# Kernel optimization log

Hardware: AMD Instinct MI355X
Metric: run time of the kernel (lower is better)

Reference implementation:

```python
import jax, jax.numpy as jnp
import numpy as np

INPUT_DIM = 64
INNER_DIM = 64
BATCH = 32768


def setup_inputs() -> dict:
    key = jax.random.key(0)
    ks = jax.random.split(key, 9)
    D, I = INPUT_DIM, INNER_DIM
    s1 = 1.0  # Linear(1, inner): fan_in=1
    s2 = 1.0 / np.sqrt(I)
    sg1 = 1.0 / np.sqrt(D * I)
    sg2 = 1.0 / np.sqrt(I)
    return {
        "x": jax.random.normal(ks[0], (BATCH, D), dtype=jnp.float32),
        # per-feature psi params, stacked over feature dim D
        "W1": jax.random.uniform(ks[1], (D, I), jnp.float32, -s1, s1),   # Linear(1, inner) weight
        "b1": jax.random.uniform(ks[2], (D, I), jnp.float32, -s1, s1),
        "W2": jax.random.uniform(ks[3], (D, I, I), jnp.float32, -s2, s2),  # Linear(inner, inner)
        "b2": jax.random.uniform(ks[4], (D, I), jnp.float32, -s2, s2),
        # g params
        "Wg1": jax.random.uniform(ks[5], (D * I, I), jnp.float32, -sg1, sg1),
        "bg1": jax.random.uniform(ks[6], (I,), jnp.float32, -sg1, sg1),
        "Wg2": jax.random.uniform(ks[7], (I, 1), jnp.float32, -sg2, sg2),
        "bg2": jax.random.uniform(ks[8], (1,), jnp.float32, -sg2, sg2),
    }


def reference(x, W1, b1, W2, b2, Wg1, bg1, Wg2, bg2):
    B = x.shape[0]
    # all psi_i first layers as one broadcasted outer product: [B, D, I]
    h = jnp.tanh(x[:, :, None] * W1[None, :, :] + b1[None, :, :])
    # per-feature second Linear(inner, inner): batched matmul over D
    psi = jnp.einsum("bdi,dio->bdo", h, W2) + b2[None, :, :]
    psi_concat = psi.reshape(B, -1)  # [B, D*I] == torch.cat over features
    hg = jnp.tanh(psi_concat @ Wg1 + bg1)
    out = hg @ Wg2 + bg2  # [B, 1]
    return out
```

## Files before the change

### kernel.cpp

```cpp
#include <hip/hip_runtime.h>
#include <stdint.h>

#define BATCH 32768
#define TANH_C 2.8853900817779268f

typedef __attribute__((ext_vector_type(8))) short short8;
typedef __attribute__((ext_vector_type(4))) float f32x4;
typedef __attribute__((ext_vector_type(16))) float f32x16;
typedef __attribute__((ext_vector_type(4))) unsigned int u32x4;

__device__ __forceinline__ uint16_t bf16_rtne(float f) {
    union { float f; uint32_t u; } v; v.f = f;
    uint32_t u = v.u;
    u += 0x7fffu + ((u >> 16) & 1u);
    return (uint16_t)(u >> 16);
}

#if defined(__has_builtin)
#if __has_builtin(__builtin_amdgcn_cvt_pk_bf16_f32)
#define HAVE_CVT_PK_BF16 1
#endif
#endif

__device__ __forceinline__ uint32_t pack2_bf16(float a, float b) {
#ifdef HAVE_CVT_PK_BF16
    auto v = __builtin_amdgcn_cvt_pk_bf16_f32(a, b);
    uint32_t r; __builtin_memcpy(&r, &v, 4); return r;
#else
    return (uint32_t)bf16_rtne(a) | ((uint32_t)bf16_rtne(b) << 16);
#endif
}

__device__ __forceinline__ uint32_t tanh2_pack(float a, float b) {
    float ea = __builtin_amdgcn_exp2f(a);
    float eb = __builtin_amdgcn_exp2f(b);
    float da = 1.0f + ea, db = 1.0f + eb;
    float ir = __builtin_amdgcn_rcpf(da * db);
    float ha = fmaf(-2.0f * db, ir, 1.0f);
    float hb = fmaf(-2.0f * da, ir, 1.0f);
    return pack2_bf16(ha, hb);
}

__device__ __forceinline__ float fast_tanh(float x) {
    float e = __builtin_amdgcn_exp2f(x * TANH_C);
    return 1.0f - 2.0f * __builtin_amdgcn_rcpf(1.0f + e);
}

__global__ __launch_bounds__(512) void kol_pack(const float* __restrict__ W2,
                                                const float* __restrict__ Wg1,
                                                const float* __restrict__ b2,
                                                uint16_t* __restrict__ Bp,
                                                float* __restrict__ cgpart) {
    __shared__ __align__(16) float w2t[64 * 65];
    __shared__ __align__(16) float g1s[64 * 64];

    const int t = threadIdx.x;
    const int d = blockIdx.x;

    for (int f = t * 4; f < 4096; f += 2048) {
        float4 v = *(const float4*)&W2[(size_t)d * 4096 + f];
        int j = f >> 6, o = f & 63;
        w2t[(o + 0) * 65 + j] = v.x;
        w2t[(o + 1) * 65 + j] = v.y;
        w2t[(o + 2) * 65 + j] = v.z;
        w2t[(o + 3) * 65 + j] = v.w;
        *(float4*)&g1s[f] = *(const float4*)&Wg1[(size_t)d * 4096 + f];
    }
    __syncthreads();

    const int jg = t >> 6;
    const int n  = t & 63;
    float acc[8];
#pragma unroll
    for (int i = 0; i < 8; ++i) acc[i] = 0.f;

#pragma unroll 4
    for (int o = 0; o < 64; ++o) {
        float g = g1s[o * 64 + n];
        const float* w = &w2t[o * 65 + jg * 8];
#pragma unroll
        for (int jj = 0; jj < 8; ++jj) acc[jj] = fmaf(w[jj], g, acc[jj]);
    }

    u32x4 pk;
    pk.x = pack2_bf16(acc[0], acc[1]);
    pk.y = pack2_bf16(acc[2], acc[3]);
    pk.z = pack2_bf16(acc[4], acc[5]);
    pk.w = pack2_bf16(acc[6], acc[7]);
    int off = ((d * 4 + (jg >> 1)) * 2 + (n >> 5)) * 64 + ((jg & 1) << 5) + (n & 31);
    ((u32x4*)Bp)[off] = pk;

    if (t < 64) {
        float a = 0.f;
        const float* b2d = &b2[(size_t)d * 64];
#pragma unroll 4
        for (int o = 0; o < 64; ++o)
            a = fmaf(b2d[o], g1s[o * 64 + t], a);
        cgpart[d * 64 + t] = a;
    }
}

__global__ __launch_bounds__(256) void kol_reduce_cg(const float* __restrict__ cgpart,
                                                     const float* __restrict__ bg1,
                                                     float* __restrict__ cg) {
    __shared__ float red[4][64];
    const int t = threadIdx.x;
    const int n = t & 63, seg = t >> 6;
    float a = 0.f;
#pragma unroll 4
    for (int d = seg * 16; d < seg * 16 + 16; ++d)
        a += cgpart[d * 64 + n];
    red[seg][n] = a;
    __syncthreads();
    if (t < 64)
        cg[n] = bg1[n] + red[0][n] + red[1][n] + red[2][n] + red[3][n];
}

__global__ __launch_bounds__(512, 4) void kol_main(
    const float* __restrict__ x, const float* __restrict__ W1, const float* __restrict__ b1,
    const uint16_t* __restrict__ Bp, const float* __restrict__ cg,
    const float* __restrict__ Wg2, const float* __restrict__ bg2f,
    float* __restrict__ out) {
    __shared__ __align__(16) float smem[12544];
    float* xs  = smem;
    float* w1s = smem + 4352;
    float* b1s = smem + 8448;

    const int tid = threadIdx.x;
    const int wave = tid >> 6, lane = tid & 63;
    const int nn = lane & 31, hi = lane >> 5;
    const int rg = wave & 1, kq = wave >> 1;
    const int rowbase = blockIdx.x * 64;

#pragma unroll
    for (int ff = 0; ff < 2; ++ff) {
        int f = tid * 4 + ff * 2048;
        int r = f >> 6, c = f & 63;
        float4 v = *(const float4*)&x[(size_t)(rowbase + r) * 64 + c];
        v.x *= TANH_C; v.y *= TANH_C; v.z *= TANH_C; v.w *= TANH_C;
        *(float4*)&xs[r * 68 + c] = v;
        *(float4*)&w1s[f] = *(const float4*)&W1[f];
        float4 b = *(const float4*)&b1[f];
        b.x *= TANH_C; b.y *= TANH_C; b.z *= TANH_C; b.w *= TANH_C;
        *(float4*)&b1s[f] = b;
    }
    __syncthreads();

    f32x16 acc0 = {0.f}, acc1 = {0.f};
#pragma unroll
    for (int i = 0; i < 16; ++i) { acc0[i] = 0.f; acc1[i] = 0.f; }

    const u32x4* bp = (const u32x4*)Bp + lane;
    const float* xcol = &xs[(rg * 32 + nn) * 68];

#pragma unroll 2
    for (int dd = 0; dd < 16; ++dd) {
        const int d = kq * 16 + dd;
        const u32x4* bfp = bp + (size_t)d * 512;
        u32x4 bfr[8];
#pragma unroll
        for (int i = 0; i < 8; ++i) bfr[i] = bfp[i * 64];

        const float xv = xcol[d];
        short8 afr[4];
#pragma unroll
        for (int c = 0; c < 4; ++c) {
            const float* wq = &w1s[d * 64 + c * 16 + hi * 8];
            const float* bq = &b1s[d * 64 + c * 16 + hi * 8];
            float4 w0 = *(const float4*)&wq[0];
            float4 w1v = *(const float4*)&wq[4];
            float4 b0 = *(const float4*)&bq[0];
            float4 b1v = *(const float4*)&bq[4];
            union { short8 s; uint32_t u[4]; } a;
            a.u[0] = tanh2_pack(fmaf(xv, w0.x, b0.x), fmaf(xv, w0.y, b0.y));
            a.u[1] = tanh2_pack(fmaf(xv, w0.z, b0.z), fmaf(xv, w0.w, b0.w));
            a.u[2] = tanh2_pack(fmaf(xv, w1v.x, b1v.x), fmaf(xv, w1v.y, b1v.y));
            a.u[3] = tanh2_pack(fmaf(xv, w1v.z, b1v.z), fmaf(xv, w1v.w, b1v.w));
            afr[c] = a.s;
        }
#pragma unroll
        for (int c = 0; c < 4; ++c) {
            union { u32x4 u; short8 s; } b0c, b1c;
            b0c.u = bfr[c * 2 + 0];
            b1c.u = bfr[c * 2 + 1];
            acc0 = __builtin_amdgcn_mfma_f32_32x32x16_bf16(afr[c], b0c.s, acc0, 0, 0, 0);
            acc1 = __builtin_amdgcn_mfma_f32_32x32x16_bf16(afr[c], b1c.s, acc1, 0, 0, 0);
        }
    }

    __syncthreads();
    f32x4* cmb = (f32x4*)smem;
    if (kq != 0) {
        const int widx = (kq - 1) * 2 + rg;
#pragma unroll
        for (int s = 0; s < 8; ++s) {
            const int base = (s & 3) * 4;
            f32x4 v;
            if (s < 4) v = (f32x4){acc0[base], acc0[base + 1], acc0[base + 2], acc0[base + 3]};
            else       v = (f32x4){acc1[base], acc1[base + 1], acc1[base + 2], acc1[base + 3]};
            cmb[(s * 6 + widx) * 64 + lane] = v;
        }
    }
    __syncthreads();

    if (kq == 0) {
#pragma unroll
        for (int s = 0; s < 8; ++s) {
            const int base = (s & 3) * 4;
            f32x4 v0 = cmb[(s * 6 + 0 + rg) * 64 + lane];
            f32x4 v1 = cmb[(s * 6 + 2 + rg) * 64 + lane];
            f32x4 v2 = cmb[(s * 6 + 4 + rg) * 64 + lane];
            f32x4 v = v0 + v1 + v2;
            if (s < 4) {
#pragma unroll
                for (int i = 0; i < 4; ++i) acc0[base + i] += v[i];
            } else {
#pragma unroll
                for (int i = 0; i < 4; ++i) acc1[base + i] += v[i];
            }
        }
        const float cg0 = cg[nn],      cg1 = cg[32 + nn];
        const float wg0 = Wg2[nn],     wg1 = Wg2[32 + nn];
        const float bg2 = bg2f[0];
#pragma unroll
        for (int g = 0; g < 4; ++g) {
            float4 res;
#pragma unroll
            for (int rr = 0; rr < 4; ++rr) {
                const int r = g * 4 + rr;
                float s = wg0 * fast_tanh(acc0[r] + cg0) + wg1 * fast_tanh(acc1[r] + cg1);
                s += __shfl_xor(s, 1, 64);
                s += __shfl_xor(s, 2, 64);
                s += __shfl_xor(s, 4, 64);
                s += __shfl_xor(s, 8, 64);
                s += __shfl_xor(s, 16, 64);
                ((float*)&res)[rr] = s + bg2;
            }
            if (nn == 0)
                *(float4*)&out[rowbase + rg * 32 + 8 * g + 4 * hi] = res;
        }
    }
}

extern "C" void kernel_launch(void* const* d_in, const int* in_sizes, int n_in,
                              void* d_out, int out_size, void* d_ws, size_t ws_size,
                              hipStream_t stream) {
    const float* x   = (const float*)d_in[0];
    const float* W1  = (const float*)d_in[1];
    const float* b1  = (const float*)d_in[2];
    const float* W2  = (const float*)d_in[3];
    const float* b2  = (const float*)d_in[4];
    const float* Wg1 = (const float*)d_in[5];
    const float* bg1 = (const float*)d_in[6];
    const float* Wg2 = (const float*)d_in[7];
    const float* bg2 = (const float*)d_in[8];
    float* out = (float*)d_out;

    uint16_t* Bp  = (uint16_t*)d_ws;
    float* cg     = (float*)((char*)d_ws + 4096 * 64 * 2);
    float* cgpart = out;

    kol_pack<<<64, 512, 0, stream>>>(W2, Wg1, b2, Bp, cgpart);
    kol_reduce_cg<<<1, 256, 0, stream>>>(cgpart, bg1, cg);
    kol_main<<<BATCH / 64, 512, 0, stream>>>(x, W1, b1, Bp, cg, Wg2, bg2, out);
}
```

Baseline: 124.3 us.

## Prefetch next B fragments, use a cheaper bf16 pack, relax launch bounds

Result: no change. 122.5 us, median of 2 (-1.5%).

```diff
diff --git a/kernel.cpp b/kernel.cpp
--- a/kernel.cpp
+++ b/kernel.cpp
@@ -16,18 +16,21 @@
     return (uint16_t)(u >> 16);
 }
 
+__device__ __forceinline__ uint32_t pack2_bf16(float a, float b) {
+    return (uint32_t)bf16_rtne(a) | ((uint32_t)bf16_rtne(b) << 16);
+}
+
+__device__ __forceinline__ uint32_t pack2_bf16_fast(float a, float b) {
+    uint32_t ra = __builtin_bit_cast(uint32_t, a) + 0x8000u;
+    uint32_t rb = __builtin_bit_cast(uint32_t, b) + 0x8000u;
 #if defined(__has_builtin)
-#if __has_builtin(__builtin_amdgcn_cvt_pk_bf16_f32)
-#define HAVE_CVT_PK_BF16 1
+#if __has_builtin(__builtin_amdgcn_perm)
+    return __builtin_amdgcn_perm(rb, ra, 0x07060302u);
+#else
+    return (rb & 0xffff0000u) | (ra >> 16);
 #endif
-#endif
-
-__device__ __forceinline__ uint32_t pack2_bf16(float a, float b) {
-#ifdef HAVE_CVT_PK_BF16
-    auto v = __builtin_amdgcn_cvt_pk_bf16_f32(a, b);
-    uint32_t r; __builtin_memcpy(&r, &v, 4); return r;
 #else
-    return (uint32_t)bf16_rtne(a) | ((uint32_t)bf16_rtne(b) << 16);
+    return (rb & 0xffff0000u) | (ra >> 16);
 #endif
 }
 
@@ -38,7 +41,7 @@
     float ir = __builtin_amdgcn_rcpf(da * db);
     float ha = fmaf(-2.0f * db, ir, 1.0f);
     float hb = fmaf(-2.0f * da, ir, 1.0f);
-    return pack2_bf16(ha, hb);
+    return pack2_bf16_fast(ha, hb);
 }
 
 __device__ __forceinline__ float fast_tanh(float x) {
@@ -116,7 +119,7 @@
         cg[n] = bg1[n] + red[0][n] + red[1][n] + red[2][n] + red[3][n];
 }
 
-__global__ __launch_bounds__(512, 4) void kol_main(
+__global__ __launch_bounds__(512, 2) void kol_main(
     const float* __restrict__ x, const float* __restrict__ W1, const float* __restrict__ b1,
     const uint16_t* __restrict__ Bp, const float* __restrict__ cg,
     const float* __restrict__ Wg2, const float* __restrict__ bg2f,
@@ -146,20 +149,28 @@
     }
     __syncthreads();
 
-    f32x16 acc0 = {0.f}, acc1 = {0.f};
+    f32x16 acc0, acc1;
 #pragma unroll
     for (int i = 0; i < 16; ++i) { acc0[i] = 0.f; acc1[i] = 0.f; }
 
     const u32x4* bp = (const u32x4*)Bp + lane;
     const float* xcol = &xs[(rg * 32 + nn) * 68];
+
+    u32x4 bcur[8];
+    {
+        const u32x4* bfp0 = bp + (size_t)(kq * 16) * 512;
+#pragma unroll
+        for (int i = 0; i < 8; ++i) bcur[i] = bfp0[i * 64];
+    }
 
 #pragma unroll 2
     for (int dd = 0; dd < 16; ++dd) {
         const int d = kq * 16 + dd;
-        const u32x4* bfp = bp + (size_t)d * 512;
-        u32x4 bfr[8];
-#pragma unroll
-        for (int i = 0; i < 8; ++i) bfr[i] = bfp[i * 64];
+
+        u32x4 bnxt[8];
+        const u32x4* bfpn = bp + (size_t)(kq * 16 + ((dd + 1) & 15)) * 512;
+#pragma unroll
+        for (int i = 0; i < 8; ++i) bnxt[i] = bfpn[i * 64];
 
         const float xv = xcol[d];
         short8 afr[4];
@@ -181,11 +192,13 @@
 #pragma unroll
         for (int c = 0; c < 4; ++c) {
             union { u32x4 u; short8 s; } b0c, b1c;
-            b0c.u = bfr[c * 2 + 0];
-            b1c.u = bfr[c * 2 + 1];
+            b0c.u = bcur[c * 2 + 0];
+            b1c.u = bcur[c * 2 + 1];
             acc0 = __builtin_amdgcn_mfma_f32_32x32x16_bf16(afr[c], b0c.s, acc0, 0, 0, 0);
             acc1 = __builtin_amdgcn_mfma_f32_32x32x16_bf16(afr[c], b1c.s, acc1, 0, 0, 0);
         }
+#pragma unroll
+        for (int i = 0; i < 8; ++i) bcur[i] = bnxt[i];
     }
 
     __syncthreads();
```
